# Optimization experiments

Hardware: AMD Instinct MI355X
Metric: run time of the kernel (lower is better)

Reference implementation:

```python
import jax, jax.numpy as jnp
import numpy as np

DIM = 128
SUPPORT = 1
NL, NM, NG = 5, 20, 100
EPS_BN = 1e-5
EPS_NORM = 1e-12


def knn_idx(vertices, k):
    # vertices: (b, v, 3) -> (b, v, k) indices of k nearest (excluding self)
    sq = jnp.sum(vertices * vertices, axis=-1)  # (b, v)
    dist = -2.0 * jnp.einsum('bic,bjc->bij', vertices, vertices) + sq[:, :, None] + sq[:, None, :]
    _, idx = jax.lax.top_k(-dist, k + 1)  # smallest distances
    return idx[:, :, 1:]


def gather_nbr(t, idx):
    # t: (b, v, c), idx: (b, v, n) -> (b, v, n, c)
    b = t.shape[0]
    return t[jnp.arange(b)[:, None, None], idx]


def conv_layer(idx, vertices, fmap, W, bias, dirs):
    # idx: (b,v,n); fmap: (b,v,DIM); W: (DIM,(S+1)*DIM); bias: ((S+1)*DIM,); dirs: (3,S*DIM)
    nbrs = gather_nbr(vertices, idx)                      # (b,v,n,3)
    d = nbrs - vertices[:, :, None, :]
    d = d / jnp.maximum(jnp.linalg.norm(d, axis=-1, keepdims=True), EPS_NORM)
    sd = dirs / jnp.maximum(jnp.linalg.norm(dirs, axis=0, keepdims=True), EPS_NORM)
    theta = jax.nn.relu(jnp.einsum('bvnc,ck->bvnk', d, sd))  # (b,v,n,S*DIM)
    fo = fmap @ W + bias                                   # (b,v,(S+1)*DIM)
    center = fo[..., :DIM]
    supp = gather_nbr(fo[..., DIM:], idx)                  # (b,v,n,S*DIM)
    b_, v_, n_ = idx.shape
    act = (theta * supp).reshape(b_, v_, n_, SUPPORT, DIM)
    act = jnp.max(act, axis=2).sum(axis=2)                 # max over neighbors, sum over supports
    return center + act                                    # (b,v,DIM)


def bn_relu(x, gamma, beta):
    # training-mode BatchNorm1d over (batch, points) per channel, then ReLU
    mu = jnp.mean(x, axis=(0, 1))
    var = jnp.var(x, axis=(0, 1))
    return jax.nn.relu((x - mu) * jax.lax.rsqrt(var + EPS_BN) * gamma + beta)


def setup_inputs() -> dict:
    key = jax.random.key(0)
    ks = jax.random.split(key, 8)
    B, V = 2, 1024
    return {
        'vertices': jax.random.normal(ks[0], (B, V, 3), jnp.float32),
        'x': jax.random.normal(ks[1], (B, V, DIM), jnp.float32),
        'conv_W': jax.random.normal(ks[2], (6, DIM, (SUPPORT + 1) * DIM), jnp.float32) * 0.05,
        'conv_b': jax.random.normal(ks[3], (6, (SUPPORT + 1) * DIM), jnp.float32) * 0.05,
        'conv_dirs': jax.random.normal(ks[4], (6, 3, SUPPORT * DIM), jnp.float32),
        'bn_gamma': jnp.ones((6, DIM), jnp.float32),
        'bn_beta': jnp.zeros((6, DIM), jnp.float32),
        'down_W': jax.random.normal(ks[5], (3 * DIM, 2 * DIM), jnp.float32) * 0.05,
        'down_b': jax.random.normal(ks[6], (2 * DIM,), jnp.float32) * 0.05,
    }


def reference(vertices, x, conv_W, conv_b, conv_dirs, bn_gamma, bn_beta, down_W, down_b):
    il = knn_idx(vertices, NL)
    im = knn_idx(vertices, NM)
    ig = knn_idx(vertices, NG)
    # param index order: 0=l, 1=m0, 2=m1, 3=g0, 4=g1, 5=g2 (g2 unused, per source bug)
    fl = bn_relu(conv_layer(il, vertices, x, conv_W[0], conv_b[0], conv_dirs[0]), bn_gamma[0], bn_beta[0])
    fm = bn_relu(conv_layer(im, vertices, x, conv_W[1], conv_b[1], conv_dirs[1]), bn_gamma[1], bn_beta[1])
    fm = bn_relu(conv_layer(im, vertices, fm, conv_W[2], conv_b[2], conv_dirs[2]), bn_gamma[2], bn_beta[2])
    fg = bn_relu(conv_layer(ig, vertices, x, conv_W[3], conv_b[3], conv_dirs[3]), bn_gamma[3], bn_beta[3])
    fg = bn_relu(conv_layer(ig, vertices, fg, conv_W[4], conv_b[4], conv_dirs[4]), bn_gamma[4], bn_beta[4])
    # source reuses conv_g0 / bn_g0 for the third global layer
    fg = bn_relu(conv_layer(ig, vertices, fg, conv_W[3], conv_b[3], conv_dirs[3]), bn_gamma[3], bn_beta[3])
    out = jnp.concatenate([fl, fm, fg], axis=2)            # (b, v, 3*DIM)
    return jax.nn.relu(out @ down_W + down_b)              # (b, v, 2*DIM)
```

## Files before the change

### kernel.cpp

```cpp
#include <hip/hip_runtime.h>

__device__ __forceinline__ void gemm_body(
    const float* __restrict__ in, const float* __restrict__ st,
    const float* __restrict__ gm, const float* __restrict__ bt,
    const float* __restrict__ W, const float* __restrict__ bi,
    float* __restrict__ out, int rb, void* smemv)
{
    float* rows  = (float*)smemv;
    float* scale = rows + 1024;
    float* shift = scale + 128;
    int t = threadIdx.x;
    if (t < 128) {
        float sc = 1.0f, sf = 0.0f;
        if (st) {
            float mu  = st[t] * (1.0f/2048.0f);
            float var = st[128+t] * (1.0f/2048.0f) - mu*mu;
            sc = rsqrtf(var + 1e-5f) * gm[t];
            sf = bt[t] - mu*sc;
        }
        scale[t] = sc; shift[t] = sf;
    }
    __syncthreads();
    int r0 = rb * 8;
    {
        float4 v = ((const float4*)(in + r0*128))[t];
        if (st) {
            int c4 = (t & 31) << 2;
            v.x = fmaxf(v.x*scale[c4  ] + shift[c4  ], 0.0f);
            v.y = fmaxf(v.y*scale[c4+1] + shift[c4+1], 0.0f);
            v.z = fmaxf(v.z*scale[c4+2] + shift[c4+2], 0.0f);
            v.w = fmaxf(v.w*scale[c4+3] + shift[c4+3], 0.0f);
        }
        ((float4*)rows)[t] = v;
    }
    __syncthreads();
    int cb = t & 63, rp = (t >> 6) << 1;
    const float* a0r = rows + rp*128;
    const float* a1r = a0r + 128;
    const float4* W4 = (const float4*)W;
    float4 acc0 = make_float4(0.f,0.f,0.f,0.f);
    float4 acc1 = make_float4(0.f,0.f,0.f,0.f);
    #pragma unroll 4
    for (int k = 0; k < 128; k += 4) {
        float4 a0 = *(const float4*)(a0r + k);
        float4 a1 = *(const float4*)(a1r + k);
        float4 w;
        w = W4[(k+0)*64+cb];
        acc0.x += a0.x*w.x; acc0.y += a0.x*w.y; acc0.z += a0.x*w.z; acc0.w += a0.x*w.w;
        acc1.x += a1.x*w.x; acc1.y += a1.x*w.y; acc1.z += a1.x*w.z; acc1.w += a1.x*w.w;
        w = W4[(k+1)*64+cb];
        acc0.x += a0.y*w.x; acc0.y += a0.y*w.y; acc0.z += a0.y*w.z; acc0.w += a0.y*w.w;
        acc1.x += a1.y*w.x; acc1.y += a1.y*w.y; acc1.z += a1.y*w.z; acc1.w += a1.y*w.w;
        w = W4[(k+2)*64+cb];
        acc0.x += a0.z*w.x; acc0.y += a0.z*w.y; acc0.z += a0.z*w.z; acc0.w += a0.z*w.w;
        acc1.x += a1.z*w.x; acc1.y += a1.z*w.y; acc1.z += a1.z*w.z; acc1.w += a1.z*w.w;
        w = W4[(k+3)*64+cb];
        acc0.x += a0.w*w.x; acc0.y += a0.w*w.y; acc0.z += a0.w*w.z; acc0.w += a0.w*w.w;
        acc1.x += a1.w*w.x; acc1.y += a1.w*w.y; acc1.z += a1.w*w.z; acc1.w += a1.w*w.w;
    }
    float4 b4 = ((const float4*)bi)[cb];
    acc0.x += b4.x; acc0.y += b4.y; acc0.z += b4.z; acc0.w += b4.w;
    acc1.x += b4.x; acc1.y += b4.y; acc1.z += b4.z; acc1.w += b4.w;
    ((float4*)out)[(r0+rp  )*64 + cb] = acc0;
    ((float4*)out)[(r0+rp+1)*64 + cb] = acc1;
}

__global__ void k1_kernel(const float* __restrict__ verts, const float* __restrict__ dirs,
                          const float* __restrict__ x,
                          const float* __restrict__ convW, const float* __restrict__ convB,
                          int* __restrict__ idxout, float* __restrict__ sdn,
                          float* __restrict__ st, float* __restrict__ fo)
{
    __shared__ __align__(16) char smem[20544];
    int t = threadIdx.x;
    int blk = blockIdx.x;

    if (blk >= 1280) {
        if (blk == 1286) {
            for (int i = t; i < 768; i += 256) {
                int l = i >> 7, k = i & 127;
                float a = dirs[l*384 + k];
                float b = dirs[l*384 + 128 + k];
                float c = dirs[l*384 + 256 + k];
                float nrm = sqrtf(a*a + b*b + c*c);
                float inv = 1.0f / fmaxf(nrm, 1e-12f);
                sdn[l*384 + k]       = a*inv;
                sdn[l*384 + 128 + k] = b*inv;
                sdn[l*384 + 256 + k] = c*inv;
            }
        } else {
            st[(blk - 1280)*256 + t] = 0.0f;
        }
        return;
    }
    if (blk >= 512) {
        int g = blk - 512;
        int s = g >> 8, rb = g & 255;
        int wi = (s==0) ? 0 : (s==1) ? 1 : 3;
        gemm_body(x, (const float*)0, (const float*)0, (const float*)0,
                  convW + wi*32768, convB + wi*256, fo + s*524288, rb, smem);
        return;
    }

    float* xs  = (float*)smem;
    float* ys  = xs + 1024;
    float* zs  = ys + 1024;
    float* sqs = zs + 1024;
    unsigned int* histBase = (unsigned int*)(smem + 16384);
    unsigned int* selBase  = (unsigned int*)(smem + 20480);

    int w = t >> 6;
    int l = t & 63;
    int vglob = blk*4 + w;
    int b = vglob >> 10;
    int v = vglob & 1023;
    unsigned long long* keys = (unsigned long long*)smem + w*256;
    unsigned int* hist = histBase + w*256;
    unsigned int* sel  = selBase + w*4;

    const float* vb = verts + b * 3072;
    for (int i = t; i < 1024; i += 256) {
        float xx = vb[i*3+0], yy = vb[i*3+1], zz = vb[i*3+2];
        xs[i] = xx; ys[i] = yy; zs[i] = zz;
        sqs[i] = xx*xx + yy*yy + zz*zz;
    }
    __syncthreads();

    float cx = xs[v], cy = ys[v], cz = zs[v], csq = sqs[v];
    unsigned long long K16[16];
    #pragma unroll
    for (int q = 0; q < 16; ++q) {
        int j = q*64 + l;
        float dot = cx*xs[j] + cy*ys[j] + cz*zs[j];
        float d = -2.0f*dot + csq + sqs[j];
        unsigned int u = __float_as_uint(d);
        u = (u & 0x80000000u) ? ~u : (u | 0x80000000u);
        K16[q] = (((unsigned long long)u) << 32) | (unsigned long long)j;
    }
    #pragma unroll
    for (int i = 0; i < 4; ++i) hist[l*4 + i] = 0u;
    __syncthreads();

    #pragma unroll
    for (int q = 0; q < 16; ++q)
        atomicAdd(&hist[(unsigned int)(K16[q] >> 56)], 1u);
    __syncthreads();

    {
        unsigned int h0 = hist[l*4], h1 = hist[l*4+1], h2 = hist[l*4+2], h3 = hist[l*4+3];
        unsigned int c1 = h0, c2 = h0+h1, c3 = h0+h1+h2, T = c3+h3;
        unsigned int xacc = T;
        #pragma unroll
        for (int off = 1; off < 64; off <<= 1) {
            unsigned int y = __shfl_up(xacc, off, 64);
            if (l >= off) xacc += y;
        }
        unsigned int P = xacc - T;
        unsigned int ex[4] = {P, P+c1, P+c2, P+c3};
        unsigned int hh[4] = {h0, h1, h2, h3};
        #pragma unroll
        for (int i = 0; i < 4; ++i) {
            if (ex[i] < 101u && ex[i] + hh[i] >= 101u) {
                sel[0] = (unsigned int)(l*4 + i);
                sel[1] = 101u - ex[i];
            }
        }
    }
    __syncthreads();
    unsigned int P8 = sel[0], rank2 = sel[1];
    #pragma unroll
    for (int i = 0; i < 4; ++i) hist[l*4 + i] = 0u;
    __syncthreads();

    #pragma unroll
    for (int q = 0; q < 16; ++q)
        if ((unsigned int)(K16[q] >> 56) == P8)
            atomicAdd(&hist[(unsigned int)(K16[q] >> 48) & 0xFFu], 1u);
    __syncthreads();

    {
        unsigned int h0 = hist[l*4], h1 = hist[l*4+1], h2 = hist[l*4+2], h3 = hist[l*4+3];
        unsigned int c1 = h0, c2 = h0+h1, c3 = h0+h1+h2, T = c3+h3;
        unsigned int xacc = T;
        #pragma unroll
        for (int off = 1; off < 64; off <<= 1) {
            unsigned int y = __shfl_up(xacc, off, 64);
            if (l >= off) xacc += y;
        }
        unsigned int P = xacc - T;
        unsigned int ex[4] = {P, P+c1, P+c2, P+c3};
        unsigned int hh[4] = {h0, h1, h2, h3};
        #pragma unroll
        for (int i = 0; i < 4; ++i) {
            if (ex[i] < rank2 && ex[i] + hh[i] >= rank2) {
                sel[2] = (P8 << 8) | (unsigned int)(l*4 + i);
                sel[3] = 0u;
            }
        }
    }
    __syncthreads();
    unsigned int P16 = sel[2];

    #pragma unroll
    for (int q = 0; q < 16; ++q) {
        if ((unsigned int)(K16[q] >> 48) <= P16) {
            unsigned int pos = atomicAdd(&sel[3], 1u);
            if (pos < 256u) keys[pos] = K16[q];
        }
    }
    __syncthreads();
    unsigned int cnt = sel[3];

    unsigned long long K[4];
    #pragma unroll
    for (int q = 0; q < 4; ++q) {
        unsigned int e = (unsigned int)(l*4 + q);
        K[q] = (e < cnt) ? keys[e] : 0xFFFFFFFFFFFFFFFFULL;
    }

    auto cswap = [&](int qa, int qb, int k) {
        int e = (l << 2) + qa;
        bool up = ((e & k) == 0);
        unsigned long long a = K[qa], bb2 = K[qb];
        unsigned long long mn = a < bb2 ? a : bb2;
        unsigned long long mx = a < bb2 ? bb2 : a;
        K[qa] = up ? mn : mx;
        K[qb] = up ? mx : mn;
    };
    #pragma unroll
    for (int k = 2; k <= 256; k <<= 1) {
        for (int j = k >> 1; j >= 4; j >>= 1) {
            int lj = j >> 2;
            #pragma unroll
            for (int q = 0; q < 4; ++q) {
                unsigned long long other = __shfl_xor(K[q], lj, 64);
                int e = (l << 2) + q;
                bool up = ((e & k) == 0);
                bool lower = ((l & lj) == 0);
                bool takeMin = (lower == up);
                unsigned long long mn = K[q] < other ? K[q] : other;
                unsigned long long mx = K[q] < other ? other : K[q];
                K[q] = takeMin ? mn : mx;
            }
        }
        if (k >= 4) { cswap(0, 2, k); cswap(1, 3, k); }
        cswap(0, 1, k); cswap(2, 3, k);
    }

    #pragma unroll
    for (int q = 0; q < 4; ++q) {
        int e = l*4 + q;
        if (e >= 1 && e <= 100)
            idxout[vglob*100 + (e-1)] = (int)(K[q] & 0xFFFFFFFFu);
    }
}

__global__ void agg_kernel(const int* __restrict__ idx, const float* __restrict__ verts,
                           const float* __restrict__ sdn, const float* __restrict__ fo,
                           int n0, int n1, int n2, int d0, int d1, int d2,
                           float* o0, float* o1, float* o2)
{
    __shared__ float4 ds4[100];
    __shared__ int js[100];
    int slot = blockIdx.y;
    int n  = slot==0 ? n0 : slot==1 ? n1 : n2;
    int dI = slot==0 ? d0 : slot==1 ? d1 : d2;
    float* outp = slot==0 ? o0 : slot==1 ? o1 : o2;
    const float* fos = fo + slot * 524288;
    const float* sd = sdn + dI * 384;

    int r = blockIdx.x;
    int b = r >> 10;
    int t = threadIdx.x;
    if (t < n) {
        int j = idx[r*100 + t];
        js[t] = j;
        const float* pj = verts + (b*1024 + j)*3;
        const float* pv = verts + r*3;
        float dx = pj[0]-pv[0], dy = pj[1]-pv[1], dz = pj[2]-pv[2];
        float nm = sqrtf(dx*dx + dy*dy + dz*dz);
        float inv = 1.0f / fmaxf(nm, 1e-12f);
        ds4[t] = make_float4(dx*inv, dy*inv, dz*inv, 0.0f);
    }
    __syncthreads();
    float s0 = sd[t], s1 = sd[128+t], s2 = sd[256+t];
    int bb = b * 1024;
    float m = -3.0e38f;
    for (int q = 0; q < n; q += 5) {
        float th[5];
        const float* p[5];
        #pragma unroll
        for (int u = 0; u < 5; ++u) {
            float4 dq = ds4[q+u];
            th[u] = fmaxf(dq.x*s0 + dq.y*s1 + dq.z*s2, 0.0f);
            p[u] = fos + (size_t)(bb + js[q+u])*256 + 128 + t;
        }
        float vv[5];
        #pragma unroll
        for (int u = 0; u < 5; ++u) vv[u] = *p[u];
        #pragma unroll
        for (int u = 0; u < 5; ++u) m = fmaxf(m, th[u]*vv[u]);
    }
    outp[r*128 + t] = fos[r*256 + t] + m;
}

__global__ void stats_kernel(const float* p0, const float* p1, const float* p2,
                             int i0, int i1, int i2, float* stats)
{
    int slot = blockIdx.y;
    const float* p = slot==0 ? p0 : slot==1 ? p1 : p2;
    float* st = stats + (slot==0 ? i0 : slot==1 ? i1 : i2) * 256;
    __shared__ float s1[256], s2[256];
    int t = threadIdx.x, k = t & 127, half = t >> 7;
    int r0 = blockIdx.x * 128;
    float sum = 0.0f, sq = 0.0f;
    for (int s = 0; s < 64; ++s) {
        float x = p[(r0 + half + 2*s)*128 + k];
        sum += x; sq += x*x;
    }
    s1[t] = sum; s2[t] = sq;
    __syncthreads();
    if (t < 128) {
        atomicAdd(&st[k],     s1[t] + s1[t+128]);
        atomicAdd(&st[128+k], s2[t] + s2[t+128]);
    }
}

__global__ void gemm2_kernel(
    const float* inA, const float* stA, const float* gA, const float* beA,
    const float* WA, const float* biA, float* foA,
    const float* inB, const float* stB, const float* gB, const float* beB,
    const float* WB, const float* biB, float* foB)
{
    __shared__ __align__(16) char smem[5120];
    if (blockIdx.y == 0)
        gemm_body(inA, stA, gA, beA, WA, biA, foA, blockIdx.x, smem);
    else
        gemm_body(inB, stB, gB, beB, WB, biB, foB, blockIdx.x, smem);
}

__global__ void down_kernel(
    const float* __restrict__ p0, const float* __restrict__ st0,
    const float* __restrict__ g0, const float* __restrict__ be0,
    const float* __restrict__ p1, const float* __restrict__ st1,
    const float* __restrict__ g1, const float* __restrict__ be1,
    const float* __restrict__ p2, const float* __restrict__ st2,
    const float* __restrict__ g2, const float* __restrict__ be2,
    const float* __restrict__ dW, const float* __restrict__ db,
    float* __restrict__ out)
{
    __shared__ float rows[8*384];
    __shared__ float scale[384], shift[384];
    int t = threadIdx.x;
    int r0 = blockIdx.x * 8;
    for (int c = t; c < 384; c += 256) {
        int seg = c >> 7, cc = c & 127;
        const float* stp = seg==0 ? st0 : seg==1 ? st1 : st2;
        const float* g   = seg==0 ? g0  : seg==1 ? g1  : g2;
        const float* be  = seg==0 ? be0 : seg==1 ? be1 : be2;
        float mu  = stp[cc] * (1.0f/2048.0f);
        float var = stp[128+cc] * (1.0f/2048.0f) - mu*mu;
        float s = rsqrtf(var + 1e-5f) * g[cc];
        scale[c] = s;
        shift[c] = be[cc] - mu*s;
    }
    __syncthreads();
    for (int q = t; q < 768; q += 256) {
        int row = q / 96, rem = q - row*96;
        int c4 = rem << 2;
        int seg = c4 >> 7, cc = c4 & 127;
        const float* ps = seg==0 ? p0 : seg==1 ? p1 : p2;
        float4 v = *(const float4*)(ps + (r0+row)*128 + cc);
        v.x = fmaxf(v.x*scale[c4  ] + shift[c4  ], 0.0f);
        v.y = fmaxf(v.y*scale[c4+1] + shift[c4+1], 0.0f);
        v.z = fmaxf(v.z*scale[c4+2] + shift[c4+2], 0.0f);
        v.w = fmaxf(v.w*scale[c4+3] + shift[c4+3], 0.0f);
        *(float4*)&rows[row*384 + c4] = v;
    }
    __syncthreads();
    int cb = t & 63, rp = (t >> 6) << 1;
    const float* a0r = rows + rp*384;
    const float* a1r = a0r + 384;
    const float4* W4 = (const float4*)dW;
    float4 acc0 = make_float4(0.f,0.f,0.f,0.f);
    float4 acc1 = make_float4(0.f,0.f,0.f,0.f);
    #pragma unroll 4
    for (int k = 0; k < 384; k += 4) {
        float4 a0 = *(const float4*)(a0r + k);
        float4 a1 = *(const float4*)(a1r + k);
        float4 w;
        w = W4[(k+0)*64+cb];
        acc0.x += a0.x*w.x; acc0.y += a0.x*w.y; acc0.z += a0.x*w.z; acc0.w += a0.x*w.w;
        acc1.x += a1.x*w.x; acc1.y += a1.x*w.y; acc1.z += a1.x*w.z; acc1.w += a1.x*w.w;
        w = W4[(k+1)*64+cb];
        acc0.x += a0.y*w.x; acc0.y += a0.y*w.y; acc0.z += a0.y*w.z; acc0.w += a0.y*w.w;
        acc1.x += a1.y*w.x; acc1.y += a1.y*w.y; acc1.z += a1.y*w.z; acc1.w += a1.y*w.w;
        w = W4[(k+2)*64+cb];
        acc0.x += a0.z*w.x; acc0.y += a0.z*w.y; acc0.z += a0.z*w.z; acc0.w += a0.z*w.w;
        acc1.x += a1.z*w.x; acc1.y += a1.z*w.y; acc1.z += a1.z*w.z; acc1.w += a1.z*w.w;
        w = W4[(k+3)*64+cb];
        acc0.x += a0.w*w.x; acc0.y += a0.w*w.y; acc0.z += a0.w*w.z; acc0.w += a0.w*w.w;
        acc1.x += a1.w*w.x; acc1.y += a1.w*w.y; acc1.z += a1.w*w.z; acc1.w += a1.w*w.w;
    }
    float4 b4 = ((const float4*)db)[cb];
    float4 o0, o1;
    o0.x = fmaxf(acc0.x + b4.x, 0.0f); o0.y = fmaxf(acc0.y + b4.y, 0.0f);
    o0.z = fmaxf(acc0.z + b4.z, 0.0f); o0.w = fmaxf(acc0.w + b4.w, 0.0f);
    o1.x = fmaxf(acc1.x + b4.x, 0.0f); o1.y = fmaxf(acc1.y + b4.y, 0.0f);
    o1.z = fmaxf(acc1.z + b4.z, 0.0f); o1.w = fmaxf(acc1.w + b4.w, 0.0f);
    ((float4*)out)[(r0+rp  )*64 + cb] = o0;
    ((float4*)out)[(r0+rp+1)*64 + cb] = o1;
}

extern "C" void kernel_launch(void* const* d_in, const int* in_sizes, int n_in,
                              void* d_out, int out_size, void* d_ws, size_t ws_size,
                              hipStream_t stream)
{
    (void)in_sizes; (void)n_in; (void)out_size; (void)ws_size;
    const float* verts = (const float*)d_in[0];
    const float* x     = (const float*)d_in[1];
    const float* convW = (const float*)d_in[2];
    const float* convB = (const float*)d_in[3];
    const float* dirs  = (const float*)d_in[4];
    const float* gam   = (const float*)d_in[5];
    const float* bet   = (const float*)d_in[6];
    const float* dW    = (const float*)d_in[7];
    const float* db    = (const float*)d_in[8];
    float* out = (float*)d_out;

    char* ws = (char*)d_ws;
    int*   idxb = (int*)(ws);
    float* sdn  = (float*)(ws + 819200);
    float* st   = (float*)(ws + 828416);
    float* fo   = (float*)(ws + 834560);
    float* p0   = (float*)(ws + 7126016);
    float* p1   = (float*)(ws + 8174592);
    float* p2   = (float*)(ws + 9223168);
    float* p3   = (float*)(ws + 10271744);
    float* p4   = (float*)(ws + 11320320);
    float* p5   = (float*)(ws + 12368896);

    const float* nf = (const float*)0;
    float* nw = (float*)0;
    float* st0 = st,        *st1 = st + 256,  *st2 = st + 512;
    float* st3 = st + 768,  *st4 = st + 1024, *st5 = st + 1280;

    k1_kernel<<<1287, 256, 0, stream>>>(verts, dirs, x, convW, convB,
                                        idxb, sdn, st, fo);
    agg_kernel<<<dim3(2048,3), 128, 0, stream>>>(
        idxb, verts, sdn, fo, 5, 20, 100, 0, 1, 3, p0, p1, p3);
    stats_kernel<<<dim3(16,3), 256, 0, stream>>>(p0, p1, p3, 0, 1, 3, st);
    gemm2_kernel<<<dim3(256,2), 256, 0, stream>>>(
        p1, st1, gam + 128, bet + 128, convW + 65536,  convB + 512,  fo,
        p3, st3, gam + 384, bet + 384, convW + 131072, convB + 1024, fo + 524288);
    agg_kernel<<<dim3(2048,2), 128, 0, stream>>>(
        idxb, verts, sdn, fo, 20, 100, 0, 2, 4, 0, p2, p4, nw);
    stats_kernel<<<dim3(16,2), 256, 0, stream>>>(p2, p4, nf, 2, 4, 0, st);
    gemm2_kernel<<<dim3(256,1), 256, 0, stream>>>(
        p4, st4, gam + 512, bet + 512, convW + 98304, convB + 768, fo,
        nf, nf, nf, nf, nf, nf, nw);
    agg_kernel<<<dim3(2048,1), 128, 0, stream>>>(
        idxb, verts, sdn, fo, 100, 0, 0, 3, 0, 0, p5, nw, nw);
    stats_kernel<<<dim3(16,1), 256, 0, stream>>>(p5, nf, nf, 5, 0, 0, st);
    down_kernel<<<256, 256, 0, stream>>>(
        p0, st0, gam, bet,
        p2, st2, gam + 256, bet + 256,
        p5, st5, gam + 384, bet + 384,
        dW, db, out);
}
```

Before: 194.9 us.

## Fuse all stages into one cooperative persistent kernel with grid syncs

Replaces the ten separate kernel launches with a single cooperative persistent kernel of 512 blocks. Each former kernel becomes a phase, work items are distributed by grid-stride loops, and phases are separated by grid.sync(). Aggregation now packs two rows per 256-thread block. This removes launch gaps and tail effects between small kernels, at the cost of grid-wide barrier overhead, a fixed block count, and higher register and LDS pressure from the merged kernel, which can lower occupancy.

```diff
diff --git a/kernel.cpp b/kernel.cpp
--- a/kernel.cpp
+++ b/kernel.cpp
@@ -1,12 +1,17 @@
 #include <hip/hip_runtime.h>
-
-__device__ __forceinline__ void gemm_body(
+#include <hip/hip_cooperative_groups.h>
+
+namespace cg = cooperative_groups;
+
+#define GRID_BLOCKS 512
+
+__device__ __forceinline__ void do_gemm(
     const float* __restrict__ in, const float* __restrict__ st,
     const float* __restrict__ gm, const float* __restrict__ bt,
     const float* __restrict__ W, const float* __restrict__ bi,
-    float* __restrict__ out, int rb, void* smemv)
-{
-    float* rows  = (float*)smemv;
+    float* __restrict__ out, int rb, char* smemc)
+{
+    float* rows  = (float*)smemc;
     float* scale = rows + 1024;
     float* shift = scale + 128;
     int t = threadIdx.x;
@@ -65,43 +70,10 @@
     ((float4*)out)[(r0+rp+1)*64 + cb] = acc1;
 }
 
-__global__ void k1_kernel(const float* __restrict__ verts, const float* __restrict__ dirs,
-                          const float* __restrict__ x,
-                          const float* __restrict__ convW, const float* __restrict__ convB,
-                          int* __restrict__ idxout, float* __restrict__ sdn,
-                          float* __restrict__ st, float* __restrict__ fo)
-{
-    __shared__ __align__(16) char smem[20544];
-    int t = threadIdx.x;
-    int blk = blockIdx.x;
-
-    if (blk >= 1280) {
-        if (blk == 1286) {
-            for (int i = t; i < 768; i += 256) {
-                int l = i >> 7, k = i & 127;
-                float a = dirs[l*384 + k];
-                float b = dirs[l*384 + 128 + k];
-                float c = dirs[l*384 + 256 + k];
-                float nrm = sqrtf(a*a + b*b + c*c);
-                float inv = 1.0f / fmaxf(nrm, 1e-12f);
-                sdn[l*384 + k]       = a*inv;
-                sdn[l*384 + 128 + k] = b*inv;
-                sdn[l*384 + 256 + k] = c*inv;
-            }
-        } else {
-            st[(blk - 1280)*256 + t] = 0.0f;
-        }
-        return;
-    }
-    if (blk >= 512) {
-        int g = blk - 512;
-        int s = g >> 8, rb = g & 255;
-        int wi = (s==0) ? 0 : (s==1) ? 1 : 3;
-        gemm_body(x, (const float*)0, (const float*)0, (const float*)0,
-                  convW + wi*32768, convB + wi*256, fo + s*524288, rb, smem);
-        return;
-    }
-
+__device__ __forceinline__ void knn_item(
+    int blk, const float* __restrict__ verts, int* __restrict__ idxout,
+    char* smem)
+{
     float* xs  = (float*)smem;
     float* ys  = xs + 1024;
     float* zs  = ys + 1024;
@@ -109,8 +81,8 @@
     unsigned int* histBase = (unsigned int*)(smem + 16384);
     unsigned int* selBase  = (unsigned int*)(smem + 20480);
 
-    int w = t >> 6;
-    int l = t & 63;
+    int t = threadIdx.x;
+    int w = t >> 6, l = t & 63;
     int vglob = blk*4 + w;
     int b = vglob >> 10;
     int v = vglob & 1023;
@@ -255,35 +227,24 @@
     }
 }
 
-__global__ void agg_kernel(const int* __restrict__ idx, const float* __restrict__ verts,
-                           const float* __restrict__ sdn, const float* __restrict__ fo,
-                           int n0, int n1, int n2, int d0, int d1, int d2,
-                           float* o0, float* o1, float* o2)
-{
-    __shared__ float4 ds4[100];
-    __shared__ int js[100];
-    int slot = blockIdx.y;
-    int n  = slot==0 ? n0 : slot==1 ? n1 : n2;
-    int dI = slot==0 ? d0 : slot==1 ? d1 : d2;
-    float* outp = slot==0 ? o0 : slot==1 ? o1 : o2;
-    const float* fos = fo + slot * 524288;
-    const float* sd = sdn + dI * 384;
-
-    int r = blockIdx.x;
+__device__ __forceinline__ void agg_row(
+    const int* __restrict__ idx, const float* __restrict__ verts,
+    const float* __restrict__ sd, const float* __restrict__ fos, int n,
+    float* __restrict__ outp, int r, int tt, float4* ds4, int* js)
+{
     int b = r >> 10;
-    int t = threadIdx.x;
-    if (t < n) {
-        int j = idx[r*100 + t];
-        js[t] = j;
+    if (tt < n) {
+        int j = idx[r*100 + tt];
+        js[tt] = j;
         const float* pj = verts + (b*1024 + j)*3;
         const float* pv = verts + r*3;
         float dx = pj[0]-pv[0], dy = pj[1]-pv[1], dz = pj[2]-pv[2];
         float nm = sqrtf(dx*dx + dy*dy + dz*dz);
         float inv = 1.0f / fmaxf(nm, 1e-12f);
-        ds4[t] = make_float4(dx*inv, dy*inv, dz*inv, 0.0f);
-    }
-    __syncthreads();
-    float s0 = sd[t], s1 = sd[128+t], s2 = sd[256+t];
+        ds4[tt] = make_float4(dx*inv, dy*inv, dz*inv, 0.0f);
+    }
+    __syncthreads();
+    float s0 = sd[tt], s1 = sd[128+tt], s2 = sd[256+tt];
     int bb = b * 1024;
     float m = -3.0e38f;
     for (int q = 0; q < n; q += 5) {
@@ -293,7 +254,7 @@
         for (int u = 0; u < 5; ++u) {
             float4 dq = ds4[q+u];
             th[u] = fmaxf(dq.x*s0 + dq.y*s1 + dq.z*s2, 0.0f);
-            p[u] = fos + (size_t)(bb + js[q+u])*256 + 128 + t;
+            p[u] = fos + (size_t)(bb + js[q+u])*256 + 128 + tt;
         }
         float vv[5];
         #pragma unroll
@@ -301,63 +262,49 @@
         #pragma unroll
         for (int u = 0; u < 5; ++u) m = fmaxf(m, th[u]*vv[u]);
     }
-    outp[r*128 + t] = fos[r*256 + t] + m;
-}
-
-__global__ void stats_kernel(const float* p0, const float* p1, const float* p2,
-                             int i0, int i1, int i2, float* stats)
-{
-    int slot = blockIdx.y;
-    const float* p = slot==0 ? p0 : slot==1 ? p1 : p2;
-    float* st = stats + (slot==0 ? i0 : slot==1 ? i1 : i2) * 256;
-    __shared__ float s1[256], s2[256];
+    outp[r*128 + tt] = fos[r*256 + tt] + m;
+}
+
+__device__ __forceinline__ void stats_item(
+    const float* __restrict__ p, float* __restrict__ stL, int sub, char* smem)
+{
+    float* s1 = (float*)smem;
+    float* s2 = s1 + 256;
     int t = threadIdx.x, k = t & 127, half = t >> 7;
-    int r0 = blockIdx.x * 128;
+    int r0 = sub * 128;
     float sum = 0.0f, sq = 0.0f;
     for (int s = 0; s < 64; ++s) {
-        float x = p[(r0 + half + 2*s)*128 + k];
-        sum += x; sq += x*x;
+        float xv = p[(r0 + half + 2*s)*128 + k];
+        sum += xv; sq += xv*xv;
     }
     s1[t] = sum; s2[t] = sq;
     __syncthreads();
     if (t < 128) {
-        atomicAdd(&st[k],     s1[t] + s1[t+128]);
-        atomicAdd(&st[128+k], s2[t] + s2[t+128]);
-    }
-}
-
-__global__ void gemm2_kernel(
-    const float* inA, const float* stA, const float* gA, const float* beA,
-    const float* WA, const float* biA, float* foA,
-    const float* inB, const float* stB, const float* gB, const float* beB,
-    const float* WB, const float* biB, float* foB)
-{
-    __shared__ __align__(16) char smem[5120];
-    if (blockIdx.y == 0)
-        gemm_body(inA, stA, gA, beA, WA, biA, foA, blockIdx.x, smem);
-    else
-        gemm_body(inB, stB, gB, beB, WB, biB, foB, blockIdx.x, smem);
-}
-
-__global__ void down_kernel(
-    const float* __restrict__ p0, const float* __restrict__ st0,
-    const float* __restrict__ g0, const float* __restrict__ be0,
-    const float* __restrict__ p1, const float* __restrict__ st1,
-    const float* __restrict__ g1, const float* __restrict__ be1,
-    const float* __restrict__ p2, const float* __restrict__ st2,
-    const float* __restrict__ g2, const float* __restrict__ be2,
+        atomicAdd(&stL[k],     s1[t] + s1[t+128]);
+        atomicAdd(&stL[128+k], s2[t] + s2[t+128]);
+    }
+}
+
+__device__ __forceinline__ void down_item(
+    const float* __restrict__ pa, const float* __restrict__ sta,
+    const float* __restrict__ ga, const float* __restrict__ bea,
+    const float* __restrict__ pb, const float* __restrict__ stb,
+    const float* __restrict__ gb, const float* __restrict__ beb,
+    const float* __restrict__ pc, const float* __restrict__ stc,
+    const float* __restrict__ gc, const float* __restrict__ bec,
     const float* __restrict__ dW, const float* __restrict__ db,
-    float* __restrict__ out)
-{
-    __shared__ float rows[8*384];
-    __shared__ float scale[384], shift[384];
+    float* __restrict__ out, int wi, char* smem)
+{
+    float* rows  = (float*)smem;
+    float* scale = rows + 3072;
+    float* shift = scale + 384;
     int t = threadIdx.x;
-    int r0 = blockIdx.x * 8;
+    int r0 = wi * 8;
     for (int c = t; c < 384; c += 256) {
         int seg = c >> 7, cc = c & 127;
-        const float* stp = seg==0 ? st0 : seg==1 ? st1 : st2;
-        const float* g   = seg==0 ? g0  : seg==1 ? g1  : g2;
-        const float* be  = seg==0 ? be0 : seg==1 ? be1 : be2;
+        const float* stp = seg==0 ? sta : seg==1 ? stb : stc;
+        const float* g   = seg==0 ? ga  : seg==1 ? gb  : gc;
+        const float* be  = seg==0 ? bea : seg==1 ? beb : bec;
         float mu  = stp[cc] * (1.0f/2048.0f);
         float var = stp[128+cc] * (1.0f/2048.0f) - mu*mu;
         float s = rsqrtf(var + 1e-5f) * g[cc];
@@ -369,7 +316,7 @@
         int row = q / 96, rem = q - row*96;
         int c4 = rem << 2;
         int seg = c4 >> 7, cc = c4 & 127;
-        const float* ps = seg==0 ? p0 : seg==1 ? p1 : p2;
+        const float* ps = seg==0 ? pa : seg==1 ? pb : pc;
         float4 v = *(const float4*)(ps + (r0+row)*128 + cc);
         v.x = fmaxf(v.x*scale[c4  ] + shift[c4  ], 0.0f);
         v.y = fmaxf(v.y*scale[c4+1] + shift[c4+1], 0.0f);
@@ -412,6 +359,131 @@
     ((float4*)out)[(r0+rp+1)*64 + cb] = o1;
 }
 
+__global__ void mega_kernel(
+    const float* __restrict__ verts, const float* __restrict__ x,
+    const float* __restrict__ convW, const float* __restrict__ convB,
+    const float* __restrict__ dirs,  const float* __restrict__ gam,
+    const float* __restrict__ bet,   const float* __restrict__ dW,
+    const float* __restrict__ db,    float* __restrict__ out,
+    int* __restrict__ idxb, float* __restrict__ sdn,
+    float* __restrict__ st, float* __restrict__ fo, float* __restrict__ pbuf)
+{
+    cg::grid_group grid = cg::this_grid();
+    __shared__ __align__(16) char smem[20544];
+    int bid = blockIdx.x, t = threadIdx.x;
+    int h = t >> 7, tt = t & 127;
+    float4* ds4 = (float4*)smem + h*100;
+    int* js = (int*)(smem + 3200) + h*100;
+
+    for (int wi = bid; wi < 1287; wi += GRID_BLOCKS) {
+        if (wi < 512) {
+            knn_item(wi, verts, idxb, smem);
+        } else if (wi < 1280) {
+            int g = wi - 512;
+            int s = g >> 8, rb = g & 255;
+            int wsel = (s==0) ? 0 : (s==1) ? 1 : 3;
+            do_gemm(x, (const float*)0, (const float*)0, (const float*)0,
+                    convW + wsel*32768, convB + wsel*256, fo + s*524288, rb, smem);
+        } else if (wi < 1286) {
+            st[(wi - 1280)*256 + t] = 0.0f;
+        } else {
+            for (int i = t; i < 768; i += 256) {
+                int l = i >> 7, k = i & 127;
+                float a = dirs[l*384 + k];
+                float b = dirs[l*384 + 128 + k];
+                float c = dirs[l*384 + 256 + k];
+                float nrm = sqrtf(a*a + b*b + c*c);
+                float inv = 1.0f / fmaxf(nrm, 1e-12f);
+                sdn[l*384 + k]       = a*inv;
+                sdn[l*384 + 128 + k] = b*inv;
+                sdn[l*384 + 256 + k] = c*inv;
+            }
+        }
+        __syncthreads();
+    }
+    grid.sync();
+
+    for (int p = bid; p < 3072; p += GRID_BLOCKS) {
+        int item = p*2 + h;
+        int slot = item >> 11, r = item & 2047;
+        int n    = slot==0 ? 5 : slot==1 ? 20 : 100;
+        int dsel = slot==0 ? 0 : slot==1 ? 1 : 3;
+        agg_row(idxb, verts, sdn + dsel*384, fo + slot*524288, n,
+                pbuf + dsel*262144, r, tt, ds4, js);
+        __syncthreads();
+    }
+    grid.sync();
+
+    for (int wi = bid; wi < 48; wi += GRID_BLOCKS) {
+        int s = wi >> 4, sub = wi & 15;
+        int lsel = (s==0) ? 0 : (s==1) ? 1 : 3;
+        stats_item(pbuf + lsel*262144, st + lsel*256, sub, smem);
+        __syncthreads();
+    }
+    grid.sync();
+
+    for (int wi = bid; wi < 512; wi += GRID_BLOCKS) {
+        int s = wi >> 8, rb = wi & 255;
+        if (s == 0)
+            do_gemm(pbuf + 1*262144, st + 256, gam + 128, bet + 128,
+                    convW + 65536, convB + 512, fo, rb, smem);
+        else
+            do_gemm(pbuf + 3*262144, st + 768, gam + 384, bet + 384,
+                    convW + 131072, convB + 1024, fo + 524288, rb, smem);
+        __syncthreads();
+    }
+    grid.sync();
+
+    for (int p = bid; p < 2048; p += GRID_BLOCKS) {
+        int item = p*2 + h;
+        int slot = item >> 11, r = item & 2047;
+        int n    = slot==0 ? 20 : 100;
+        int dsel = slot==0 ? 2 : 4;
+        agg_row(idxb, verts, sdn + dsel*384, fo + slot*524288, n,
+                pbuf + dsel*262144, r, tt, ds4, js);
+        __syncthreads();
+    }
+    grid.sync();
+
+    for (int wi = bid; wi < 32; wi += GRID_BLOCKS) {
+        int s = wi >> 4, sub = wi & 15;
+        int lsel = (s==0) ? 2 : 4;
+        stats_item(pbuf + lsel*262144, st + lsel*256, sub, smem);
+        __syncthreads();
+    }
+    grid.sync();
+
+    for (int wi = bid; wi < 256; wi += GRID_BLOCKS) {
+        do_gemm(pbuf + 4*262144, st + 1024, gam + 512, bet + 512,
+                convW + 98304, convB + 768, fo, wi, smem);
+        __syncthreads();
+    }
+    grid.sync();
+
+    for (int p = bid; p < 1024; p += GRID_BLOCKS) {
+        int item = p*2 + h;
+        int r = item & 2047;
+        agg_row(idxb, verts, sdn + 3*384, fo, 100,
+                pbuf + 5*262144, r, tt, ds4, js);
+        __syncthreads();
+    }
+    grid.sync();
+
+    for (int wi = bid; wi < 16; wi += GRID_BLOCKS) {
+        stats_item(pbuf + 5*262144, st + 1280, wi, smem);
+        __syncthreads();
+    }
+    grid.sync();
+
+    for (int wi = bid; wi < 256; wi += GRID_BLOCKS) {
+        down_item(pbuf,            st,        gam,       bet,
+                  pbuf + 2*262144, st + 512,  gam + 256, bet + 256,
+                  pbuf + 5*262144, st + 1280, gam + 384, bet + 384,
+                  dW, db, out, wi, smem);
+        __syncthreads();
+    }
+}
+
 extern "C" void kernel_launch(void* const* d_in, const int* in_sizes, int n_in,
                               void* d_out, int out_size, void* d_ws, size_t ws_size,
                               hipStream_t stream)
@@ -433,38 +505,13 @@
     float* sdn  = (float*)(ws + 819200);
     float* st   = (float*)(ws + 828416);
     float* fo   = (float*)(ws + 834560);
-    float* p0   = (float*)(ws + 7126016);
-    float* p1   = (float*)(ws + 8174592);
-    float* p2   = (float*)(ws + 9223168);
-    float* p3   = (float*)(ws + 10271744);
-    float* p4   = (float*)(ws + 11320320);
-    float* p5   = (float*)(ws + 12368896);
-
-    const float* nf = (const float*)0;
-    float* nw = (float*)0;
-    float* st0 = st,        *st1 = st + 256,  *st2 = st + 512;
-    float* st3 = st + 768,  *st4 = st + 1024, *st5 = st + 1280;
-
-    k1_kernel<<<1287, 256, 0, stream>>>(verts, dirs, x, convW, convB,
-                                        idxb, sdn, st, fo);
-    agg_kernel<<<dim3(2048,3), 128, 0, stream>>>(
-        idxb, verts, sdn, fo, 5, 20, 100, 0, 1, 3, p0, p1, p3);
-    stats_kernel<<<dim3(16,3), 256, 0, stream>>>(p0, p1, p3, 0, 1, 3, st);
-    gemm2_kernel<<<dim3(256,2), 256, 0, stream>>>(
-        p1, st1, gam + 128, bet + 128, convW + 65536,  convB + 512,  fo,
-        p3, st3, gam + 384, bet + 384, convW + 131072, convB + 1024, fo + 524288);
-    agg_kernel<<<dim3(2048,2), 128, 0, stream>>>(
-        idxb, verts, sdn, fo, 20, 100, 0, 2, 4, 0, p2, p4, nw);
-    stats_kernel<<<dim3(16,2), 256, 0, stream>>>(p2, p4, nf, 2, 4, 0, st);
-    gemm2_kernel<<<dim3(256,1), 256, 0, stream>>>(
-        p4, st4, gam + 512, bet + 512, convW + 98304, convB + 768, fo,
-        nf, nf, nf, nf, nf, nf, nw);
-    agg_kernel<<<dim3(2048,1), 128, 0, stream>>>(
-        idxb, verts, sdn, fo, 100, 0, 0, 3, 0, 0, p5, nw, nw);
-    stats_kernel<<<dim3(16,1), 256, 0, stream>>>(p5, nf, nf, 5, 0, 0, st);
-    down_kernel<<<256, 256, 0, stream>>>(
-        p0, st0, gam, bet,
-        p2, st2, gam + 256, bet + 256,
-        p5, st5, gam + 384, bet + 384,
-        dW, db, out);
-}
+    float* pbuf = (float*)(ws + 7126016);
+
+    void* args[] = {
+        (void*)&verts, (void*)&x, (void*)&convW, (void*)&convB, (void*)&dirs,
+        (void*)&gam, (void*)&bet, (void*)&dW, (void*)&db, (void*)&out,
+        (void*)&idxb, (void*)&sdn, (void*)&st, (void*)&fo, (void*)&pbuf
+    };
+    hipLaunchCooperativeKernel((const void*)mega_kernel,
+                               dim3(GRID_BLOCKS), dim3(256), args, 0, stream);
+}
```

Measured after the change: 772.5 us. 3.96x slower.

## Stage weight chunks in shared memory for GEMMs and process two rows per agg block

Applied to the files above, without the earlier changes.

The small GEMM bodies (conv and down projection) now cooperatively load 16-row chunks of the weight matrix into shared memory before computing, where each thread previously read its weights straight from global memory. Separately, the aggregation kernel handles two vertices per 256-thread block instead of one per 128-thread block, halving the block count. The staging adds barriers per chunk and more LDS per block, which may cut occupancy, and the weights were probably already served from cache.

```diff
diff --git a/kernel.cpp b/kernel.cpp
--- a/kernel.cpp
+++ b/kernel.cpp
@@ -1,13 +1,14 @@
 #include <hip/hip_runtime.h>
 
-__device__ __forceinline__ void gemm_body(
+__device__ __forceinline__ void do_gemm(
     const float* __restrict__ in, const float* __restrict__ st,
     const float* __restrict__ gm, const float* __restrict__ bt,
     const float* __restrict__ W, const float* __restrict__ bi,
-    float* __restrict__ out, int rb, void* smemv)
-{
-    float* rows  = (float*)smemv;
-    float* scale = rows + 1024;
+    float* __restrict__ out, int rb, char* smemc)
+{
+    float* rows  = (float*)smemc;
+    float* wch   = rows + 1024;
+    float* scale = wch + 4096;
     float* shift = scale + 128;
     int t = threadIdx.x;
     if (t < 128) {
@@ -33,30 +34,38 @@
         }
         ((float4*)rows)[t] = v;
     }
-    __syncthreads();
     int cb = t & 63, rp = (t >> 6) << 1;
     const float* a0r = rows + rp*128;
     const float* a1r = a0r + 128;
     const float4* W4 = (const float4*)W;
+    float4* wch4 = (float4*)wch;
     float4 acc0 = make_float4(0.f,0.f,0.f,0.f);
     float4 acc1 = make_float4(0.f,0.f,0.f,0.f);
-    #pragma unroll 4
-    for (int k = 0; k < 128; k += 4) {
-        float4 a0 = *(const float4*)(a0r + k);
-        float4 a1 = *(const float4*)(a1r + k);
-        float4 w;
-        w = W4[(k+0)*64+cb];
-        acc0.x += a0.x*w.x; acc0.y += a0.x*w.y; acc0.z += a0.x*w.z; acc0.w += a0.x*w.w;
-        acc1.x += a1.x*w.x; acc1.y += a1.x*w.y; acc1.z += a1.x*w.z; acc1.w += a1.x*w.w;
-        w = W4[(k+1)*64+cb];
-        acc0.x += a0.y*w.x; acc0.y += a0.y*w.y; acc0.z += a0.y*w.z; acc0.w += a0.y*w.w;
-        acc1.x += a1.y*w.x; acc1.y += a1.y*w.y; acc1.z += a1.y*w.z; acc1.w += a1.y*w.w;
-        w = W4[(k+2)*64+cb];
-        acc0.x += a0.z*w.x; acc0.y += a0.z*w.y; acc0.z += a0.z*w.z; acc0.w += a0.z*w.w;
-        acc1.x += a1.z*w.x; acc1.y += a1.z*w.y; acc1.z += a1.z*w.z; acc1.w += a1.z*w.w;
-        w = W4[(k+3)*64+cb];
-        acc0.x += a0.w*w.x; acc0.y += a0.w*w.y; acc0.z += a0.w*w.z; acc0.w += a0.w*w.w;
-        acc1.x += a1.w*w.x; acc1.y += a1.w*w.y; acc1.z += a1.w*w.z; acc1.w += a1.w*w.w;
+    for (int c = 0; c < 8; ++c) {
+        __syncthreads();
+        #pragma unroll
+        for (int i = 0; i < 4; ++i)
+            wch4[t + 256*i] = W4[c*1024 + t + 256*i];
+        __syncthreads();
+        int kb = c*16;
+        #pragma unroll
+        for (int k = 0; k < 16; k += 4) {
+            float4 a0 = *(const float4*)(a0r + kb + k);
+            float4 a1 = *(const float4*)(a1r + kb + k);
+            float4 w;
+            w = wch4[(k+0)*64+cb];
+            acc0.x += a0.x*w.x; acc0.y += a0.x*w.y; acc0.z += a0.x*w.z; acc0.w += a0.x*w.w;
+            acc1.x += a1.x*w.x; acc1.y += a1.x*w.y; acc1.z += a1.x*w.z; acc1.w += a1.x*w.w;
+            w = wch4[(k+1)*64+cb];
+            acc0.x += a0.y*w.x; acc0.y += a0.y*w.y; acc0.z += a0.y*w.z; acc0.w += a0.y*w.w;
+            acc1.x += a1.y*w.x; acc1.y += a1.y*w.y; acc1.z += a1.y*w.z; acc1.w += a1.y*w.w;
+            w = wch4[(k+2)*64+cb];
+            acc0.x += a0.z*w.x; acc0.y += a0.z*w.y; acc0.z += a0.z*w.z; acc0.w += a0.z*w.w;
+            acc1.x += a1.z*w.x; acc1.y += a1.z*w.y; acc1.z += a1.z*w.z; acc1.w += a1.z*w.w;
+            w = wch4[(k+3)*64+cb];
+            acc0.x += a0.w*w.x; acc0.y += a0.w*w.y; acc0.z += a0.w*w.z; acc0.w += a0.w*w.w;
+            acc1.x += a1.w*w.x; acc1.y += a1.w*w.y; acc1.z += a1.w*w.z; acc1.w += a1.w*w.w;
+        }
     }
     float4 b4 = ((const float4*)bi)[cb];
     acc0.x += b4.x; acc0.y += b4.y; acc0.z += b4.z; acc0.w += b4.w;
@@ -71,7 +80,7 @@
                           int* __restrict__ idxout, float* __restrict__ sdn,
                           float* __restrict__ st, float* __restrict__ fo)
 {
-    __shared__ __align__(16) char smem[20544];
+    __shared__ __align__(16) char smem[21504];
     int t = threadIdx.x;
     int blk = blockIdx.x;
 
@@ -97,8 +106,8 @@
         int g = blk - 512;
         int s = g >> 8, rb = g & 255;
         int wi = (s==0) ? 0 : (s==1) ? 1 : 3;
-        gemm_body(x, (const float*)0, (const float*)0, (const float*)0,
-                  convW + wi*32768, convB + wi*256, fo + s*524288, rb, smem);
+        do_gemm(x, (const float*)0, (const float*)0, (const float*)0,
+                convW + wi*32768, convB + wi*256, fo + s*524288, rb, smem);
         return;
     }
 
@@ -109,8 +118,7 @@
     unsigned int* histBase = (unsigned int*)(smem + 16384);
     unsigned int* selBase  = (unsigned int*)(smem + 20480);
 
-    int w = t >> 6;
-    int l = t & 63;
+    int w = t >> 6, l = t & 63;
     int vglob = blk*4 + w;
     int b = vglob >> 10;
     int v = vglob & 1023;
@@ -260,8 +268,8 @@
                            int n0, int n1, int n2, int d0, int d1, int d2,
                            float* o0, float* o1, float* o2)
 {
-    __shared__ float4 ds4[100];
-    __shared__ int js[100];
+    __shared__ float4 ds4s[200];
+    __shared__ int jss[200];
     int slot = blockIdx.y;
     int n  = slot==0 ? n0 : slot==1 ? n1 : n2;
     int dI = slot==0 ? d0 : slot==1 ? d1 : d2;
@@ -269,21 +277,25 @@
     const float* fos = fo + slot * 524288;
     const float* sd = sdn + dI * 384;
 
-    int r = blockIdx.x;
+    int t = threadIdx.x;
+    int h = t >> 7, tt = t & 127;
+    float4* ds4 = ds4s + h*100;
+    int* js = jss + h*100;
+    int r = blockIdx.x*2 + h;
     int b = r >> 10;
-    int t = threadIdx.x;
-    if (t < n) {
-        int j = idx[r*100 + t];
-        js[t] = j;
+
+    if (tt < n) {
+        int j = idx[r*100 + tt];
+        js[tt] = j;
         const float* pj = verts + (b*1024 + j)*3;
         const float* pv = verts + r*3;
         float dx = pj[0]-pv[0], dy = pj[1]-pv[1], dz = pj[2]-pv[2];
         float nm = sqrtf(dx*dx + dy*dy + dz*dz);
         float inv = 1.0f / fmaxf(nm, 1e-12f);
-        ds4[t] = make_float4(dx*inv, dy*inv, dz*inv, 0.0f);
-    }
-    __syncthreads();
-    float s0 = sd[t], s1 = sd[128+t], s2 = sd[256+t];
+        ds4[tt] = make_float4(dx*inv, dy*inv, dz*inv, 0.0f);
+    }
+    __syncthreads();
+    float s0 = sd[tt], s1 = sd[128+tt], s2 = sd[256+tt];
     int bb = b * 1024;
     float m = -3.0e38f;
     for (int q = 0; q < n; q += 5) {
@@ -293,7 +305,7 @@
         for (int u = 0; u < 5; ++u) {
             float4 dq = ds4[q+u];
             th[u] = fmaxf(dq.x*s0 + dq.y*s1 + dq.z*s2, 0.0f);
-            p[u] = fos + (size_t)(bb + js[q+u])*256 + 128 + t;
+            p[u] = fos + (size_t)(bb + js[q+u])*256 + 128 + tt;
         }
         float vv[5];
         #pragma unroll
@@ -301,7 +313,7 @@
         #pragma unroll
         for (int u = 0; u < 5; ++u) m = fmaxf(m, th[u]*vv[u]);
     }
-    outp[r*128 + t] = fos[r*256 + t] + m;
+    outp[r*128 + tt] = fos[r*256 + tt] + m;
 }
 
 __global__ void stats_kernel(const float* p0, const float* p1, const float* p2,
@@ -332,11 +344,11 @@
     const float* inB, const float* stB, const float* gB, const float* beB,
     const float* WB, const float* biB, float* foB)
 {
-    __shared__ __align__(16) char smem[5120];
+    __shared__ __align__(16) char smem[21504];
     if (blockIdx.y == 0)
-        gemm_body(inA, stA, gA, beA, WA, biA, foA, blockIdx.x, smem);
+        do_gemm(inA, stA, gA, beA, WA, biA, foA, blockIdx.x, smem);
     else
-        gemm_body(inB, stB, gB, beB, WB, biB, foB, blockIdx.x, smem);
+        do_gemm(inB, stB, gB, beB, WB, biB, foB, blockIdx.x, smem);
 }
 
 __global__ void down_kernel(
@@ -350,6 +362,7 @@
     float* __restrict__ out)
 {
     __shared__ float rows[8*384];
+    __shared__ float wch[16*256];
     __shared__ float scale[384], shift[384];
     int t = threadIdx.x;
     int r0 = blockIdx.x * 8;
@@ -377,30 +390,38 @@
         v.w = fmaxf(v.w*scale[c4+3] + shift[c4+3], 0.0f);
         *(float4*)&rows[row*384 + c4] = v;
     }
-    __syncthreads();
     int cb = t & 63, rp = (t >> 6) << 1;
     const float* a0r = rows + rp*384;
     const float* a1r = a0r + 384;
     const float4* W4 = (const float4*)dW;
+    float4* wch4 = (float4*)wch;
     float4 acc0 = make_float4(0.f,0.f,0.f,0.f);
     float4 acc1 = make_float4(0.f,0.f,0.f,0.f);
-    #pragma unroll 4
-    for (int k = 0; k < 384; k += 4) {
-        float4 a0 = *(const float4*)(a0r + k);
-        float4 a1 = *(const float4*)(a1r + k);
-        float4 w;
-        w = W4[(k+0)*64+cb];
-        acc0.x += a0.x*w.x; acc0.y += a0.x*w.y; acc0.z += a0.x*w.z; acc0.w += a0.x*w.w;
-        acc1.x += a1.x*w.x; acc1.y += a1.x*w.y; acc1.z += a1.x*w.z; acc1.w += a1.x*w.w;
-        w = W4[(k+1)*64+cb];
-        acc0.x += a0.y*w.x; acc0.y += a0.y*w.y; acc0.z += a0.y*w.z; acc0.w += a0.y*w.w;
-        acc1.x += a1.y*w.x; acc1.y += a1.y*w.y; acc1.z += a1.y*w.z; acc1.w += a1.y*w.w;
-        w = W4[(k+2)*64+cb];
-        acc0.x += a0.z*w.x; acc0.y += a0.z*w.y; acc0.z += a0.z*w.z; acc0.w += a0.z*w.w;
-        acc1.x += a1.z*w.x; acc1.y += a1.z*w.y; acc1.z += a1.z*w.z; acc1.w += a1.z*w.w;
-        w = W4[(k+3)*64+cb];
-        acc0.x += a0.w*w.x; acc0.y += a0.w*w.y; acc0.z += a0.w*w.z; acc0.w += a0.w*w.w;
-        acc1.x += a1.w*w.x; acc1.y += a1.w*w.y; acc1.z += a1.w*w.z; acc1.w += a1.w*w.w;
+    for (int c = 0; c < 24; ++c) {
+        __syncthreads();
+        #pragma unroll
+        for (int i = 0; i < 4; ++i)
+            wch4[t + 256*i] = W4[c*1024 + t + 256*i];
+        __syncthreads();
+        int kb = c*16;
+        #pragma unroll
+        for (int k = 0; k < 16; k += 4) {
+            float4 a0 = *(const float4*)(a0r + kb + k);
+            float4 a1 = *(const float4*)(a1r + kb + k);
+            float4 w;
+            w = wch4[(k+0)*64+cb];
+            acc0.x += a0.x*w.x; acc0.y += a0.x*w.y; acc0.z += a0.x*w.z; acc0.w += a0.x*w.w;
+            acc1.x += a1.x*w.x; acc1.y += a1.x*w.y; acc1.z += a1.x*w.z; acc1.w += a1.x*w.w;
+            w = wch4[(k+1)*64+cb];
+            acc0.x += a0.y*w.x; acc0.y += a0.y*w.y; acc0.z += a0.y*w.z; acc0.w += a0.y*w.w;
+            acc1.x += a1.y*w.x; acc1.y += a1.y*w.y; acc1.z += a1.y*w.z; acc1.w += a1.y*w.w;
+            w = wch4[(k+2)*64+cb];
+            acc0.x += a0.z*w.x; acc0.y += a0.z*w.y; acc0.z += a0.z*w.z; acc0.w += a0.z*w.w;
+            acc1.x += a1.z*w.x; acc1.y += a1.z*w.y; acc1.z += a1.z*w.z; acc1.w += a1.z*w.w;
+            w = wch4[(k+3)*64+cb];
+            acc0.x += a0.w*w.x; acc0.y += a0.w*w.y; acc0.z += a0.w*w.z; acc0.w += a0.w*w.w;
+            acc1.x += a1.w*w.x; acc1.y += a1.w*w.y; acc1.z += a1.w*w.z; acc1.w += a1.w*w.w;
+        }
     }
     float4 b4 = ((const float4*)db)[cb];
     float4 o0, o1;
@@ -447,19 +468,19 @@
 
     k1_kernel<<<1287, 256, 0, stream>>>(verts, dirs, x, convW, convB,
                                         idxb, sdn, st, fo);
-    agg_kernel<<<dim3(2048,3), 128, 0, stream>>>(
+    agg_kernel<<<dim3(1024,3), 256, 0, stream>>>(
         idxb, verts, sdn, fo, 5, 20, 100, 0, 1, 3, p0, p1, p3);
     stats_kernel<<<dim3(16,3), 256, 0, stream>>>(p0, p1, p3, 0, 1, 3, st);
     gemm2_kernel<<<dim3(256,2), 256, 0, stream>>>(
         p1, st1, gam + 128, bet + 128, convW + 65536,  convB + 512,  fo,
         p3, st3, gam + 384, bet + 384, convW + 131072, convB + 1024, fo + 524288);
-    agg_kernel<<<dim3(2048,2), 128, 0, stream>>>(
+    agg_kernel<<<dim3(1024,2), 256, 0, stream>>>(
         idxb, verts, sdn, fo, 20, 100, 0, 2, 4, 0, p2, p4, nw);
     stats_kernel<<<dim3(16,2), 256, 0, stream>>>(p2, p4, nf, 2, 4, 0, st);
     gemm2_kernel<<<dim3(256,1), 256, 0, stream>>>(
         p4, st4, gam + 512, bet + 512, convW + 98304, convB + 768, fo,
         nf, nf, nf, nf, nf, nf, nw);
-    agg_kernel<<<dim3(2048,1), 128, 0, stream>>>(
+    agg_kernel<<<dim3(1024,1), 256, 0, stream>>>(
         idxb, verts, sdn, fo, 100, 0, 0, 3, 0, 0, p5, nw, nw);
     stats_kernel<<<dim3(16,1), 256, 0, stream>>>(p5, nf, nf, 5, 0, 0, st);
     down_kernel<<<256, 256, 0, stream>>>(
```

Result: faster. 189.1 us (-3.0%).
